# Kernel optimization log

Hardware: AMD Instinct MI355X
Metric: run time of the kernel (lower is better)

The kernel has to match this reference:

```python
import jax, jax.numpy as jnp
import numpy as np

N = 50000          # nodes
E = 800000         # edges
F_IN = 128         # node_features
HID = 128          # hidden_dim
OUT = 64           # out_channels
TOP = 4            # top_features (gate channels)
EXP = 3            # experts
G = 64             # num graphs in batch
TEMP = 101.0       # 100 - 0/(200*0.01) + final_temperature(1.0) at batch counter 0


def setup_inputs() -> dict:
    key = jax.random.key(0)
    ks = jax.random.split(key, 12)
    s = 0.08  # weight init scale
    x = jax.random.normal(ks[0], (N, F_IN), jnp.float32)
    top_features = jax.random.normal(ks[1], (N, TOP), jnp.float32)
    edge_index = jax.random.randint(ks[2], (2, E), 0, N, dtype=jnp.int64)
    batch = jnp.sort(jax.random.randint(ks[3], (N,), 0, G, dtype=jnp.int64))
    W0 = jax.random.normal(ks[4], (EXP, F_IN, HID), jnp.float32) * s
    b0 = jax.random.normal(ks[5], (EXP, HID), jnp.float32) * s
    Wg0 = jax.random.normal(ks[6], (EXP, TOP), jnp.float32) * s
    W1 = jax.random.normal(ks[7], (EXP, HID, HID), jnp.float32) * s
    b1 = jax.random.normal(ks[8], (EXP, HID), jnp.float32) * s
    Wg1 = jax.random.normal(ks[9], (EXP, TOP), jnp.float32) * s
    Wf = jax.random.normal(ks[10], (HID, OUT), jnp.float32) * s
    bf = jax.random.normal(ks[11], (OUT,), jnp.float32) * s
    return {"x": x, "top_features": top_features, "edge_index": edge_index,
            "batch": batch, "W0": W0, "b0": b0, "Wg0": Wg0,
            "W1": W1, "b1": b1, "Wg1": Wg1, "Wf": Wf, "bf": bf}


def reference(x, top_features, edge_index, batch, W0, b0, Wg0, W1, b1, Wg1, Wf, bf):
    # GCN with self-loops and symmetric normalization (PyG GCNConv default)
    sl = jnp.arange(N, dtype=edge_index.dtype)
    src = jnp.concatenate([edge_index[0], sl])
    dst = jnp.concatenate([edge_index[1], sl])
    deg = jax.ops.segment_sum(jnp.ones_like(src, jnp.float32), dst, num_segments=N)
    dinv = jax.lax.rsqrt(deg)  # deg >= 1 thanks to self loops
    norm = dinv[src] * dinv[dst]  # [E+N]

    def camoe_layer(h, W, b, Wg):
        # gate: softmax over experts at temperature TEMP
        gate = jax.nn.softmax((top_features @ Wg.T) / TEMP, axis=-1)  # [N, EXP]
        out = jnp.zeros((N, W.shape[2]), h.dtype)
        for e in range(EXP):  # small fixed expert loop (keeps peak memory low)
            he = h @ W[e]                                            # [N, HID]
            agg = jax.ops.segment_sum(he[src] * norm[:, None], dst, num_segments=N)
            out = out + gate[:, e:e + 1] * jax.nn.relu(agg + b[e])
        return out

    h = camoe_layer(x, W0, b0, Wg0)
    # F.dropout before last layer: eval mode -> identity
    h = camoe_layer(h, W1, b1, Wg1)

    # global mean pool over graphs
    sums = jax.ops.segment_sum(h, batch, num_segments=G)             # [G, HID]
    cnt = jax.ops.segment_sum(jnp.ones((N,), h.dtype), batch, num_segments=G)
    pooled = sums / jnp.maximum(cnt, 1.0)[:, None]
    return pooled @ Wf + bf                                          # [G, OUT]
```

## Files before the change

kernel.cpp:

```cpp
#include <hip/hip_runtime.h>
#include <hip/hip_bf16.h>

#define HID 128
#define EXP 3
#define TOP 4
#define OUTC 64
#define SLOTC 64

typedef __bf16 bf16x8 __attribute__((ext_vector_type(8)));
typedef float f32x16 __attribute__((ext_vector_type(16)));
typedef float f32x2 __attribute__((ext_vector_type(2)));

#define GLDS_STRIDE 272
#define OUT_STRIDE 132

__device__ __forceinline__ unsigned int pack4_fp8(float a, float b, float c, float d) {
    int v = 0;
    v = __builtin_amdgcn_cvt_pk_fp8_f32(a, b, v, false);
    v = __builtin_amdgcn_cvt_pk_fp8_f32(c, d, v, true);
    return (unsigned int)v;
}

__device__ __forceinline__ void unpack4_fp8(unsigned int v, float* out) {
    f32x2 lo = __builtin_amdgcn_cvt_pk_f32_fp8((int)v, false);
    f32x2 hi = __builtin_amdgcn_cvt_pk_f32_fp8((int)v, true);
    out[0] = lo[0]; out[1] = lo[1]; out[2] = hi[0]; out[3] = hi[1];
}

__device__ __forceinline__ void add16_fp8(uint4 a, float* acc) {
    unsigned int q[4] = {a.x, a.y, a.z, a.w};
#pragma unroll
    for (int k = 0; k < 4; ++k) {
        float f[4];
        unpack4_fp8(q[k], f);
#pragma unroll
        for (int j = 0; j < 4; ++j) acc[k * 4 + j] += f[j];
    }
}


__global__ __launch_bounds__(256) void mega0_kernel(
        const int* __restrict__ src, const int* __restrict__ dst,
        int* __restrict__ cnt, int* __restrict__ slots, int E,
        const float* __restrict__ tf, const float* __restrict__ Wg0,
        const float* __restrict__ Wg1, float* __restrict__ gates,
        const int* __restrict__ batch, int* __restrict__ gstart,
        const float* __restrict__ W0, const float* __restrict__ W1,
        __bf16* __restrict__ ph0, __bf16* __restrict__ ph1,
        int N, int G, int nFill, int nGate) {
    int b = blockIdx.x;
    int t = threadIdx.x;

    if (b < nFill) {
        int slice = b & 7;
        int base = (b >> 3) * 2048 + t * 8;
        if (base < E) {
            if (base + 8 <= E) {
                int4 d0 = *(const int4*)(dst + base);
                int4 d1 = *(const int4*)(dst + base + 4);
                int dv[8] = {d0.x, d0.y, d0.z, d0.w, d1.x, d1.y, d1.z, d1.w};
#pragma unroll
                for (int k = 0; k < 8; ++k) {
                    int d = dv[k];
                    if (((d >> 6) & 7) != slice) continue;
                    int s = src[base + k];
                    int p = atomicAdd(&cnt[d], 1);
                    if (p < SLOTC) slots[(size_t)d * SLOTC + p] = s;
                }
            } else {
                for (int i = base; i < E; ++i) {
                    int d = dst[i];
                    if (((d >> 6) & 7) != slice) continue;
                    int s = src[i];
                    int p = atomicAdd(&cnt[d], 1);
                    if (p < SLOTC) slots[(size_t)d * SLOTC + p] = s;
                }
            }
        }
        return;
    }
    b -= nFill;
    if (b < nGate) {
        int n = b * 256 + t;
        if (n >= N) return;
        float4 tv = *(const float4*)(tf + (size_t)n * TOP);
        const float* Wg[2] = {Wg0, Wg1};
#pragma unroll
        for (int l = 0; l < 2; ++l) {
            float lg[EXP];
#pragma unroll
            for (int e = 0; e < EXP; ++e) {
                const float* w = Wg[l] + e * TOP;
                lg[e] = (tv.x * w[0] + tv.y * w[1] + tv.z * w[2] + tv.w * w[3]) * (1.0f / 101.0f);
            }
            float m = fmaxf(lg[0], fmaxf(lg[1], lg[2]));
            float e0 = expf(lg[0] - m), e1 = expf(lg[1] - m), e2 = expf(lg[2] - m);
            float inv = 1.0f / (e0 + e1 + e2);
            gates[n * 6 + l * 3 + 0] = e0 * inv;
            gates[n * 6 + l * 3 + 1] = e1 * inv;
            gates[n * 6 + l * 3 + 2] = e2 * inv;
        }
        return;
    }
    b -= nGate;
    if (b == 0) {
        int g = t;
        if (g > G) return;
        if (g == G) { gstart[G] = N; return; }
        int lo = 0, hi = N;
        while (lo < hi) {
            int mid = (lo + hi) >> 1;
            if (batch[mid] < g) lo = mid + 1; else hi = mid;
        }
        gstart[g] = lo;
        return;
    }
    b -= 1;
    int job = b * 4 + (t >> 6);
    if (job >= 192) return;
    int l = t & 63;
    int layer = job / 96;
    int rem = job % 96;
    int e = rem / 32;
    int s = (rem % 32) / 4;
    int c = rem % 4;
    const float* W = layer ? W1 : W0;
    __bf16* ph = layer ? ph1 : ph0;
    size_t dstbase = (size_t)((((e * 8 + s) * 4 + c) * 64 + l)) * 8;
    int kbase = s * 16 + (l >> 5) * 8;
    int ncol = c * 32 + (l & 31);
#pragma unroll
    for (int j = 0; j < 8; ++j) {
        float w = W[(size_t)e * (HID * HID) + (size_t)(kbase + j) * HID + ncol];
        ph[dstbase + j] = (__bf16)w;
    }
}


__global__ __launch_bounds__(256) void prep2_kernel(const float* __restrict__ x,
                                                    unsigned int* __restrict__ x8,
                                                    const int* __restrict__ cnt, int N) {
    int i = blockIdx.x * 256 + threadIdx.x;
    int total16 = N * (HID / 16);
    if (i >= total16) return;
    int n = i >> 3;
    float dn = rsqrtf((float)cnt[n] + 1.0f);
    const float4* xp = (const float4*)x + (size_t)i * 4;
    float4 v0 = xp[0], v1 = xp[1], v2 = xp[2], v3 = xp[3];
    uint4 o;
    o.x = pack4_fp8(v0.x * dn, v0.y * dn, v0.z * dn, v0.w * dn);
    o.y = pack4_fp8(v1.x * dn, v1.y * dn, v1.z * dn, v1.w * dn);
    o.z = pack4_fp8(v2.x * dn, v2.y * dn, v2.z * dn, v2.w * dn);
    o.w = pack4_fp8(v3.x * dn, v3.y * dn, v3.z * dn, v3.w * dn);
    ((uint4*)x8)[i] = o;
}


__global__ __launch_bounds__(512, 4) void fused_layer_kernel(
        const unsigned char* __restrict__ h8in,
        const __bf16* __restrict__ wpkh,
        const float* __restrict__ bias, const float* __restrict__ gates, int gate_off,
        const int* __restrict__ cnt, const int* __restrict__ slots,
        unsigned char* __restrict__ hout8,
        const int* __restrict__ batch, float* __restrict__ pooled, int N) {
    __shared__ char lds[64 * OUT_STRIDE * 4];
    int tid = threadIdx.x;
    int row0 = blockIdx.x * 64;

    {
        int r = tid >> 3;
        int part = tid & 7;
        int n = row0 + r;
        float acc[16];
#pragma unroll
        for (int j = 0; j < 16; ++j) acc[j] = 0.f;
        if (n < N) {
            const unsigned char* hb = h8in + part * 16;
            int degt = cnt[n];
            int deg = min(degt, SLOTC);
            float dn = rsqrtf((float)degt + 1.0f);
            uint4 v = *(const uint4*)(hb + (size_t)n * HID);
            {
                unsigned int q[4] = {v.x, v.y, v.z, v.w};
#pragma unroll
                for (int k = 0; k < 4; ++k) {
                    float f[4];
                    unpack4_fp8(q[k], f);
#pragma unroll
                    for (int j = 0; j < 4; ++j) acc[k * 4 + j] = f[j];
                }
            }
            const int* sl = slots + (size_t)n * SLOTC;
            int i = 0;
            for (; i + 4 <= deg; i += 4) {
                int4 sv = *(const int4*)(sl + i);
                uint4 a0 = *(const uint4*)(hb + (size_t)sv.x * HID);
                uint4 a1 = *(const uint4*)(hb + (size_t)sv.y * HID);
                uint4 a2 = *(const uint4*)(hb + (size_t)sv.z * HID);
                uint4 a3 = *(const uint4*)(hb + (size_t)sv.w * HID);
                add16_fp8(a0, acc);
                add16_fp8(a1, acc);
                add16_fp8(a2, acc);
                add16_fp8(a3, acc);
            }
            for (; i < deg; ++i) {
                uint4 a0 = *(const uint4*)(hb + (size_t)sl[i] * HID);
                add16_fp8(a0, acc);
            }
#pragma unroll
            for (int j = 0; j < 16; ++j) acc[j] *= dn;
        }
        char* drow = lds + r * GLDS_STRIDE + part * 32;
        bf16x8 h0, h1;
#pragma unroll
        for (int j = 0; j < 8; ++j) { h0[j] = (__bf16)acc[j]; h1[j] = (__bf16)acc[8 + j]; }
        *(bf16x8*)drow = h0;
        *(bf16x8*)(drow + 16) = h1;
    }
    __syncthreads();

    int lane = tid & 63;
    int wave = tid >> 6;
    int m = lane & 31;
    int g = lane >> 5;
    int rhalf = wave & 1;
    int cq = wave >> 1;
    const char* arow = lds + (rhalf * 32 + m) * GLDS_STRIDE + g * 16;
    int rowbase = row0 + rhalf * 32 + 4 * g;

    float F[16];
#pragma unroll
    for (int r = 0; r < 16; ++r) F[r] = 0.f;

    for (int e = 0; e < EXP; ++e) {
        f32x16 acc;
#pragma unroll
        for (int r = 0; r < 16; ++r) acc[r] = 0.f;

#pragma unroll
        for (int s = 0; s < 8; ++s) {
            bf16x8 Ah = *(const bf16x8*)(arow + s * 32);
            bf16x8 Bh = *(const bf16x8*)(wpkh + (size_t)(((e * 8 + s) * 4 + cq) * 64 + lane) * 8);
            acc = __builtin_amdgcn_mfma_f32_32x32x16_bf16(Ah, Bh, acc, 0, 0, 0);
        }
        float gt[16];
#pragma unroll
        for (int r = 0; r < 16; ++r) {
            int rr = rowbase + (r & 3) + 8 * (r >> 2);
            gt[r] = (rr < N) ? gates[(size_t)rr * 6 + gate_off + e] : 0.f;
        }
        float bb = bias[e * HID + cq * 32 + m];
#pragma unroll
        for (int r = 0; r < 16; ++r)
            F[r] += gt[r] * fmaxf(acc[r] + bb, 0.f);
    }

    __syncthreads();
    float* lds32 = (float*)lds;
    {
        int colg = cq * 32 + m;
#pragma unroll
        for (int r = 0; r < 16; ++r) {
            int lr = rhalf * 32 + 4 * g + (r & 3) + 8 * (r >> 2);
            lds32[lr * OUT_STRIDE + colg] = F[r];
        }
    }
    __syncthreads();

    if (hout8) {
#pragma unroll
        for (int it = 0; it < 4; ++it) {
            int id = tid + it * 512;
            int r = id >> 5;
            int c4 = id & 31;
            int gr = row0 + r;
            if (gr < N) {
                float dr = rsqrtf((float)cnt[gr] + 1.0f);
                const float* src = &lds32[r * OUT_STRIDE + c4 * 4];
                *(unsigned int*)(hout8 + (size_t)gr * HID + c4 * 4) =
                    pack4_fp8(src[0] * dr, src[1] * dr, src[2] * dr, src[3] * dr);
            }
        }
    }
    if (pooled) {
        int col = tid & 127;
        int rbase = (tid >> 7) * 16;
        int cur = -1;
        float acc = 0.f;
        for (int r = 0; r < 16; ++r) {
            int gr = row0 + rbase + r;
            if (gr >= N) break;
            int gb = batch[gr];
            if (gb != cur) {
                if (cur >= 0) atomicAdd(&pooled[cur * HID + col], acc);
                acc = 0.f;
                cur = gb;
            }
            acc += lds32[(rbase + r) * OUT_STRIDE + col];
        }
        if (cur >= 0) atomicAdd(&pooled[cur * HID + col], acc);
    }
}


__global__ __launch_bounds__(64) void final_kernel(const float* __restrict__ pooled,
                                                   const int* __restrict__ gstart,
                                                   const float* __restrict__ Wf,
                                                   const float* __restrict__ bf,
                                                   float* __restrict__ out) {
    __shared__ float ps[HID];
    int g = blockIdx.x;
    int o = threadIdx.x;
    float invc = 1.0f / fmaxf((float)(gstart[g + 1] - gstart[g]), 1.0f);
    ps[o] = pooled[g * HID + o] * invc;
    ps[o + 64] = pooled[g * HID + o + 64] * invc;
    __syncthreads();
    float acc = bf[o];
#pragma unroll 8
    for (int k = 0; k < HID; ++k) acc = fmaf(ps[k], Wf[k * OUTC + o], acc);
    out[g * OUTC + o] = acc;
}


extern "C" void kernel_launch(void* const* d_in, const int* in_sizes, int n_in,
                              void* d_out, int out_size, void* d_ws, size_t ws_size,
                              hipStream_t stream) {
    const float* x   = (const float*)d_in[0];
    const float* tf  = (const float*)d_in[1];
    const int*   ei  = (const int*)d_in[2];
    const int*   bat = (const int*)d_in[3];
    const float* W0  = (const float*)d_in[4];
    const float* b0  = (const float*)d_in[5];
    const float* Wg0 = (const float*)d_in[6];
    const float* W1  = (const float*)d_in[7];
    const float* b1  = (const float*)d_in[8];
    const float* Wg1 = (const float*)d_in[9];
    const float* Wf  = (const float*)d_in[10];
    const float* bf  = (const float*)d_in[11];
    float* out = (float*)d_out;

    const int N = in_sizes[0] / HID;
    const int E = in_sizes[2] / 2;
    const int G = out_size / OUTC;

    char* p = (char*)d_ws;
    auto alloc = [&](size_t bytes) -> void* {
        void* r = (void*)p;
        p += (bytes + 255) & ~(size_t)255;
        return r;
    };
    int*           cnt    = (int*)alloc((size_t)N * 4);
    float*         pooled = (float*)alloc((size_t)G * HID * 4);
    int*           slots  = (int*)alloc((size_t)N * SLOTC * 4);
    float*         gates  = (float*)alloc((size_t)N * 6 * 4);
    unsigned char* x8     = (unsigned char*)alloc((size_t)N * HID);
    unsigned char* h8b    = (unsigned char*)alloc((size_t)N * HID);
    int*           gstart = (int*)alloc((size_t)(G + 1) * 4);
    __bf16*        wpkh0  = (__bf16*)alloc((size_t)EXP * HID * HID * 2);
    __bf16*        wpkh1  = (__bf16*)alloc((size_t)EXP * HID * HID * 2);

    const int* src = ei;
    const int* dst = ei + E;

    size_t zlen = (size_t)((char*)pooled - (char*)cnt) + (size_t)G * HID * 4;
    hipMemsetAsync(cnt, 0, zlen, stream);

    const int nFill = ((E + 2047) / 2048) * 8;
    const int nGate = (N + 255) / 256;
    const int megaBlocks = nFill + nGate + 1 + 48;

    mega0_kernel<<<megaBlocks, 256, 0, stream>>>(src, dst, cnt, slots, E,
                                                 tf, Wg0, Wg1, gates,
                                                 bat, gstart,
                                                 W0, W1, wpkh0, wpkh1,
                                                 N, G, nFill, nGate);

    const int prepBlocks = (N * (HID / 16) + 255) / 256;
    prep2_kernel<<<prepBlocks, 256, 0, stream>>>(x, (unsigned int*)x8, cnt, N);

    int gemm_blocks = (N + 63) / 64;

    fused_layer_kernel<<<gemm_blocks, 512, 0, stream>>>(x8, wpkh0, b0, gates, 0,
                                                        cnt, slots,
                                                        h8b, nullptr, nullptr, N);
    fused_layer_kernel<<<gemm_blocks, 512, 0, stream>>>(h8b, wpkh1, b1, gates, 3,
                                                        cnt, slots,
                                                        nullptr, bat, pooled, N);

    final_kernel<<<G, 64, 0, stream>>>(pooled, gstart, Wf, bf, out);
}
```

Before: 221.1 us.

## Halve rows per fused-layer block and unroll neighbor gather by eight

Each fused layer block now handles 32 rows with 256 threads instead of 64 rows with 512. Every wave computes one 32-column quarter of the output for all rows, with the LDS, epilogue and pooling indexing changed to match. The neighbor gather loop now issues eight row loads per iteration and prefetches the next eight slot indices, to raise memory-level parallelism on the irregular fp8 gathers. The trade-offs are twice as many blocks, each expert weight fragment reused across fewer rows, and a prefetch that can read slot indices past the node's degree (past the end of the slot array for a maximal-degree final node).

New measurement: 268.7 us. +21.5%, slower.

```diff
diff --git a/kernel.cpp b/kernel.cpp
--- a/kernel.cpp
+++ b/kernel.cpp
@@ -13,6 +13,7 @@
 
 #define GLDS_STRIDE 272
 #define OUT_STRIDE 132
+#define ROWS 32
 
 __device__ __forceinline__ unsigned int pack4_fp8(float a, float b, float c, float d) {
     int v = 0;
@@ -156,16 +157,16 @@
 }
 
 
-__global__ __launch_bounds__(512, 4) void fused_layer_kernel(
+__global__ __launch_bounds__(256, 4) void fused_layer_kernel(
         const unsigned char* __restrict__ h8in,
         const __bf16* __restrict__ wpkh,
         const float* __restrict__ bias, const float* __restrict__ gates, int gate_off,
         const int* __restrict__ cnt, const int* __restrict__ slots,
         unsigned char* __restrict__ hout8,
         const int* __restrict__ batch, float* __restrict__ pooled, int N) {
-    __shared__ char lds[64 * OUT_STRIDE * 4];
+    __shared__ char lds[ROWS * OUT_STRIDE * 4];
     int tid = threadIdx.x;
-    int row0 = blockIdx.x * 64;
+    int row0 = blockIdx.x * ROWS;
 
     {
         int r = tid >> 3;
@@ -192,6 +193,30 @@
             }
             const int* sl = slots + (size_t)n * SLOTC;
             int i = 0;
+            if (deg >= 8) {
+                int4 sv0 = *(const int4*)(sl);
+                int4 sv1 = *(const int4*)(sl + 4);
+                for (; i + 8 <= deg; i += 8) {
+                    uint4 a0 = *(const uint4*)(hb + (size_t)sv0.x * HID);
+                    uint4 a1 = *(const uint4*)(hb + (size_t)sv0.y * HID);
+                    uint4 a2 = *(const uint4*)(hb + (size_t)sv0.z * HID);
+                    uint4 a3 = *(const uint4*)(hb + (size_t)sv0.w * HID);
+                    uint4 a4 = *(const uint4*)(hb + (size_t)sv1.x * HID);
+                    uint4 a5 = *(const uint4*)(hb + (size_t)sv1.y * HID);
+                    uint4 a6 = *(const uint4*)(hb + (size_t)sv1.z * HID);
+                    uint4 a7 = *(const uint4*)(hb + (size_t)sv1.w * HID);
+                    sv0 = *(const int4*)(sl + i + 8);
+                    sv1 = *(const int4*)(sl + i + 12);
+                    add16_fp8(a0, acc);
+                    add16_fp8(a1, acc);
+                    add16_fp8(a2, acc);
+                    add16_fp8(a3, acc);
+                    add16_fp8(a4, acc);
+                    add16_fp8(a5, acc);
+                    add16_fp8(a6, acc);
+                    add16_fp8(a7, acc);
+                }
+            }
             for (; i + 4 <= deg; i += 4) {
                 int4 sv = *(const int4*)(sl + i);
                 uint4 a0 = *(const uint4*)(hb + (size_t)sv.x * HID);
@@ -220,13 +245,11 @@
     __syncthreads();
 
     int lane = tid & 63;
-    int wave = tid >> 6;
+    int cq = tid >> 6;
     int m = lane & 31;
     int g = lane >> 5;
-    int rhalf = wave & 1;
-    int cq = wave >> 1;
-    const char* arow = lds + (rhalf * 32 + m) * GLDS_STRIDE + g * 16;
-    int rowbase = row0 + rhalf * 32 + 4 * g;
+    const char* arow = lds + m * GLDS_STRIDE + g * 16;
+    int rowbase = row0 + 4 * g;
 
     float F[16];
 #pragma unroll
@@ -261,7 +284,7 @@
         int colg = cq * 32 + m;
 #pragma unroll
         for (int r = 0; r < 16; ++r) {
-            int lr = rhalf * 32 + 4 * g + (r & 3) + 8 * (r >> 2);
+            int lr = 4 * g + (r & 3) + 8 * (r >> 2);
             lds32[lr * OUT_STRIDE + colg] = F[r];
         }
     }
@@ -270,7 +293,7 @@
     if (hout8) {
 #pragma unroll
         for (int it = 0; it < 4; ++it) {
-            int id = tid + it * 512;
+            int id = tid + it * 256;
             int r = id >> 5;
             int c4 = id & 31;
             int gr = row0 + r;
@@ -378,12 +401,12 @@
     const int prepBlocks = (N * (HID / 16) + 255) / 256;
     prep2_kernel<<<prepBlocks, 256, 0, stream>>>(x, (unsigned int*)x8, cnt, N);
 
-    int gemm_blocks = (N + 63) / 64;
-
-    fused_layer_kernel<<<gemm_blocks, 512, 0, stream>>>(x8, wpkh0, b0, gates, 0,
+    int gemm_blocks = (N + ROWS - 1) / ROWS;
+
+    fused_layer_kernel<<<gemm_blocks, 256, 0, stream>>>(x8, wpkh0, b0, gates, 0,
                                                         cnt, slots,
                                                         h8b, nullptr, nullptr, N);
-    fused_layer_kernel<<<gemm_blocks, 512, 0, stream>>>(h8b, wpkh1, b1, gates, 3,
+    fused_layer_kernel<<<gemm_blocks, 256, 0, stream>>>(h8b, wpkh1, b1, gates, 3,
                                                         cnt, slots,
                                                         nullptr, bat, pooled, N);
 
```

## Split fused gather+GEMM into column-half aggregation kernels and separate GEMM

Applied to the files above, without the earlier changes.

The fused layer kernel is split into a standalone aggregation kernel and a GEMM kernel. The aggregation runs twice per layer, once per 64-column half of the fp8 features, which shrinks the gather working set per pass for better cache hit rates. It also prefetches the next slot indices ahead of the gather loads. The cost is an extra bf16 intermediate buffer written and read through global memory, plus two more kernel launches per layer.

Measured after the change: 252.9 us. +14.4%, slower.

```diff
diff --git a/kernel.cpp b/kernel.cpp
--- a/kernel.cpp
+++ b/kernel.cpp
@@ -156,66 +156,85 @@
 }
 
 
-__global__ __launch_bounds__(512, 4) void fused_layer_kernel(
+__global__ __launch_bounds__(256) void agg_kernel(
         const unsigned char* __restrict__ h8in,
+        const int* __restrict__ cnt, const int* __restrict__ slots,
+        __bf16* __restrict__ agg, int half, int N) {
+    int tid = threadIdx.x;
+    int r = tid >> 2;
+    int part = tid & 3;
+    int n = blockIdx.x * 64 + r;
+    if (n >= N) return;
+
+    const unsigned char* hb = h8in + half * 64 + part * 16;
+    int degt = cnt[n];
+    int deg = min(degt, SLOTC);
+    float dn = rsqrtf((float)degt + 1.0f);
+
+    float acc[16];
+    uint4 v = *(const uint4*)(hb + (size_t)n * HID);
+    {
+        unsigned int q[4] = {v.x, v.y, v.z, v.w};
+#pragma unroll
+        for (int k = 0; k < 4; ++k) {
+            float f[4];
+            unpack4_fp8(q[k], f);
+#pragma unroll
+            for (int j = 0; j < 4; ++j) acc[k * 4 + j] = f[j];
+        }
+    }
+    const int* sl = slots + (size_t)n * SLOTC;
+    int i = 0;
+    if (deg >= 4) {
+        int4 sv = *(const int4*)(sl);
+        for (; i + 4 <= deg; i += 4) {
+            uint4 a0 = *(const uint4*)(hb + (size_t)sv.x * HID);
+            uint4 a1 = *(const uint4*)(hb + (size_t)sv.y * HID);
+            uint4 a2 = *(const uint4*)(hb + (size_t)sv.z * HID);
+            uint4 a3 = *(const uint4*)(hb + (size_t)sv.w * HID);
+            sv = *(const int4*)(sl + i + 4);
+            add16_fp8(a0, acc);
+            add16_fp8(a1, acc);
+            add16_fp8(a2, acc);
+            add16_fp8(a3, acc);
+        }
+    }
+    for (; i < deg; ++i) {
+        uint4 a0 = *(const uint4*)(hb + (size_t)sl[i] * HID);
+        add16_fp8(a0, acc);
+    }
+#pragma unroll
+    for (int j = 0; j < 16; ++j) acc[j] *= dn;
+
+    __bf16* dp = agg + (size_t)n * HID + half * 64 + part * 16;
+    bf16x8 h0, h1;
+#pragma unroll
+    for (int j = 0; j < 8; ++j) { h0[j] = (__bf16)acc[j]; h1[j] = (__bf16)acc[8 + j]; }
+    *(bf16x8*)dp = h0;
+    *(bf16x8*)(dp + 8) = h1;
+}
+
+
+__global__ __launch_bounds__(512, 4) void gemm_kernel(
+        const __bf16* __restrict__ agg,
         const __bf16* __restrict__ wpkh,
         const float* __restrict__ bias, const float* __restrict__ gates, int gate_off,
-        const int* __restrict__ cnt, const int* __restrict__ slots,
+        const int* __restrict__ cnt,
         unsigned char* __restrict__ hout8,
         const int* __restrict__ batch, float* __restrict__ pooled, int N) {
     __shared__ char lds[64 * OUT_STRIDE * 4];
     int tid = threadIdx.x;
     int row0 = blockIdx.x * 64;
 
-    {
-        int r = tid >> 3;
-        int part = tid & 7;
-        int n = row0 + r;
-        float acc[16];
-#pragma unroll
-        for (int j = 0; j < 16; ++j) acc[j] = 0.f;
-        if (n < N) {
-            const unsigned char* hb = h8in + part * 16;
-            int degt = cnt[n];
-            int deg = min(degt, SLOTC);
-            float dn = rsqrtf((float)degt + 1.0f);
-            uint4 v = *(const uint4*)(hb + (size_t)n * HID);
-            {
-                unsigned int q[4] = {v.x, v.y, v.z, v.w};
-#pragma unroll
-                for (int k = 0; k < 4; ++k) {
-                    float f[4];
-                    unpack4_fp8(q[k], f);
-#pragma unroll
-                    for (int j = 0; j < 4; ++j) acc[k * 4 + j] = f[j];
-                }
-            }
-            const int* sl = slots + (size_t)n * SLOTC;
-            int i = 0;
-            for (; i + 4 <= deg; i += 4) {
-                int4 sv = *(const int4*)(sl + i);
-                uint4 a0 = *(const uint4*)(hb + (size_t)sv.x * HID);
-                uint4 a1 = *(const uint4*)(hb + (size_t)sv.y * HID);
-                uint4 a2 = *(const uint4*)(hb + (size_t)sv.z * HID);
-                uint4 a3 = *(const uint4*)(hb + (size_t)sv.w * HID);
-                add16_fp8(a0, acc);
-                add16_fp8(a1, acc);
-                add16_fp8(a2, acc);
-                add16_fp8(a3, acc);
-            }
-            for (; i < deg; ++i) {
-                uint4 a0 = *(const uint4*)(hb + (size_t)sl[i] * HID);
-                add16_fp8(a0, acc);
-            }
-#pragma unroll
-            for (int j = 0; j < 16; ++j) acc[j] *= dn;
-        }
-        char* drow = lds + r * GLDS_STRIDE + part * 32;
-        bf16x8 h0, h1;
-#pragma unroll
-        for (int j = 0; j < 8; ++j) { h0[j] = (__bf16)acc[j]; h1[j] = (__bf16)acc[8 + j]; }
-        *(bf16x8*)drow = h0;
-        *(bf16x8*)(drow + 16) = h1;
+#pragma unroll
+    for (int it = 0; it < 2; ++it) {
+        int id = tid + it * 512;
+        int r = id >> 4;
+        int c = id & 15;
+        int gr = row0 + r;
+        float4 vh = make_float4(0.f, 0.f, 0.f, 0.f);
+        if (gr < N) vh = ((const float4*)agg)[(size_t)gr * 16 + c];
+        *(float4*)(lds + r * GLDS_STRIDE + c * 16) = vh;
     }
     __syncthreads();
 
@@ -355,6 +374,7 @@
     float*         gates  = (float*)alloc((size_t)N * 6 * 4);
     unsigned char* x8     = (unsigned char*)alloc((size_t)N * HID);
     unsigned char* h8b    = (unsigned char*)alloc((size_t)N * HID);
+    __bf16*        aggbuf = (__bf16*)alloc((size_t)N * HID * 2);
     int*           gstart = (int*)alloc((size_t)(G + 1) * 4);
     __bf16*        wpkh0  = (__bf16*)alloc((size_t)EXP * HID * HID * 2);
     __bf16*        wpkh1  = (__bf16*)alloc((size_t)EXP * HID * HID * 2);
@@ -378,14 +398,17 @@
     const int prepBlocks = (N * (HID / 16) + 255) / 256;
     prep2_kernel<<<prepBlocks, 256, 0, stream>>>(x, (unsigned int*)x8, cnt, N);
 
-    int gemm_blocks = (N + 63) / 64;
-
-    fused_layer_kernel<<<gemm_blocks, 512, 0, stream>>>(x8, wpkh0, b0, gates, 0,
-                                                        cnt, slots,
-                                                        h8b, nullptr, nullptr, N);
-    fused_layer_kernel<<<gemm_blocks, 512, 0, stream>>>(h8b, wpkh1, b1, gates, 3,
-                                                        cnt, slots,
-                                                        nullptr, bat, pooled, N);
+    const int nbAgg = (N + 63) / 64;
+
+    agg_kernel<<<nbAgg, 256, 0, stream>>>(x8, cnt, slots, aggbuf, 0, N);
+    agg_kernel<<<nbAgg, 256, 0, stream>>>(x8, cnt, slots, aggbuf, 1, N);
+    gemm_kernel<<<nbAgg, 512, 0, stream>>>(aggbuf, wpkh0, b0, gates, 0, cnt,
+                                           h8b, nullptr, nullptr, N);
+
+    agg_kernel<<<nbAgg, 256, 0, stream>>>(h8b, cnt, slots, aggbuf, 0, N);
+    agg_kernel<<<nbAgg, 256, 0, stream>>>(h8b, cnt, slots, aggbuf, 1, N);
+    gemm_kernel<<<nbAgg, 512, 0, stream>>>(aggbuf, wpkh1, b1, gates, 3, cnt,
+                                           nullptr, bat, pooled, N);
 
     final_kernel<<<G, 64, 0, stream>>>(pooled, gstart, Wf, bf, out);
 }
```
